# Performance work log

Hardware: AMD Instinct MI355X
Metric: run time of the kernel (lower is better)

Reference implementation:

```python
import jax, jax.numpy as jnp
import numpy as np
from jax import lax

IN_DIM = 256
MID = IN_DIM // 2          # 128
NUM_FILTERS = 8
OUT_DIM = 256
EMBED_DIM = 256
BN_EPS = 1e-5


def star_relu(x, scale, bias):
    # StarReLU: s * relu(x)**2 + b
    return scale * jnp.square(jax.nn.relu(x)) + bias


def setup_inputs() -> dict:
    key = jax.random.key(0)
    ks = jax.random.split(key, 12)
    B, H, W = 2, 16, 16
    h, w = 128, 128
    inp = {
        "x": jax.random.normal(ks[0], (B, IN_DIM, H, W), jnp.float32),
        "y": jax.random.normal(ks[1], (B, OUT_DIM, h, w), jnp.float32),
        # feature_fuse: 1x1 conv, depthwise 3x3 conv, BatchNorm (eval-mode stats)
        "conv1_w": jax.random.normal(ks[2], (MID, IN_DIM), jnp.float32) * 0.02,
        "conv1_b": jnp.zeros((MID,), jnp.float32),
        "dw_w": jax.random.normal(ks[3], (MID, 3, 3), jnp.float32) * 0.02,
        "dw_b": jnp.zeros((MID,), jnp.float32),
        "bn_gamma": jnp.ones((MID,), jnp.float32),
        "bn_beta": jnp.zeros((MID,), jnp.float32),
        "bn_mean": jax.random.normal(ks[4], (MID,), jnp.float32) * 0.1,
        "bn_var": jax.random.uniform(ks[5], (MID,), jnp.float32, 0.5, 1.5),
        "sr1_scale": jnp.ones((1,), jnp.float32),
        "sr1_bias": jnp.zeros((1,), jnp.float32),
        # channle_expand 1x1 conv
        "ce_w": jax.random.normal(ks[6], (NUM_FILTERS, MID), jnp.float32) * 0.02,
        "ce_b": jnp.zeros((NUM_FILTERS,), jnp.float32),
        "sr2_scale": jnp.ones((1,), jnp.float32),
        "sr2_bias": jnp.zeros((1,), jnp.float32),
        "W_base": jax.random.normal(ks[7], (OUT_DIM * EMBED_DIM, NUM_FILTERS), jnp.float32) * 0.02,
    }
    return inp


def reference(x, y, conv1_w, conv1_b, dw_w, dw_b, bn_gamma, bn_beta, bn_mean,
              bn_var, sr1_scale, sr1_bias, ce_w, ce_b, sr2_scale, sr2_bias, W_base):
    B, _, fh, fw = x.shape
    b, c, h, w = y.shape
    ph, pw = h // fh, w // fw

    # feature_fuse
    t = jnp.einsum('bchw,oc->bohw', x, conv1_w) + conv1_b[None, :, None, None]
    t = lax.conv_general_dilated(
        t, dw_w[:, None, :, :], (1, 1), ((1, 1), (1, 1)),
        feature_group_count=MID,
        dimension_numbers=('NCHW', 'OIHW', 'NCHW')) + dw_b[None, :, None, None]
    t = bn_gamma[None, :, None, None] * (t - bn_mean[None, :, None, None]) \
        * lax.rsqrt(bn_var + BN_EPS)[None, :, None, None] + bn_beta[None, :, None, None]
    t = star_relu(t, sr1_scale, sr1_bias)

    # channle_expand + act -> per-location filter coefficients [b, F, fh, fw]
    wdec = star_relu(jnp.einsum('bchw,fc->bfhw', t, ce_w) + ce_b[None, :, None, None],
                     sr2_scale, sr2_bias)

    # hypernetwork: [b, E*O, fh, fw], flattened as (embed_dim, out_dim)
    Wd = jnp.einsum('bfhw,ef->behw', wdec, W_base)
    Wd = Wd.reshape(b, EMBED_DIM, OUT_DIM, fh, fw)

    # massive-group 1x1 conv == per-(batch, block) small GEMM over spatial patches
    yb = y.reshape(b, c, fh, ph, fw, pw)
    out = jnp.einsum('beoij,boipjq->beipjq', Wd, yb)  # [b, E, fh, ph, fw, pw]
    return out.reshape(b, EMBED_DIM, h, w)
```

## Files before the change

### kernel.cpp

```cpp
#include <hip/hip_runtime.h>
#include <stdint.h>

typedef unsigned short u16t;
typedef unsigned int   u32t;
typedef _Float16       h16;
typedef __attribute__((ext_vector_type(2))) _Float16 h16x2;
typedef __attribute__((ext_vector_type(8))) short    short8;
typedef __attribute__((ext_vector_type(4))) float    f32x4;

#if defined(__has_builtin)
#if __has_builtin(__builtin_amdgcn_fdot2)
#define HAVE_DOT2 1
#endif
#endif

__device__ __forceinline__ float dot2h(u32t a, u32t b, float c){
#ifdef HAVE_DOT2
  return __builtin_amdgcn_fdot2(__builtin_bit_cast(h16x2, a),
                                __builtin_bit_cast(h16x2, b), c, false);
#else
  h16x2 ha = __builtin_bit_cast(h16x2, a), hb = __builtin_bit_cast(h16x2, b);
  return c + (float)ha[0]*(float)hb[0] + (float)ha[1]*(float)hb[1];
#endif
}

__device__ __forceinline__ float bf2f(u16t h){
  union { u32t u; float f; } c; c.u = ((u32t)h) << 16; return c.f;
}
__device__ __forceinline__ u32t pk2bf(float a, float b){
  u32t ua = __builtin_bit_cast(u32t, a) + 0x8000u;
  u32t ub = __builtin_bit_cast(u32t, b) + 0x8000u;
  return __builtin_amdgcn_perm(ub, ua, 0x07060302u);
}
__device__ __forceinline__ u32t pk2h(float a, float b){
  h16x2 h = { (h16)a, (h16)b };
  return __builtin_bit_cast(u32t, h);
}

template<bool BF>
__device__ __forceinline__ float ldv(const void* p, size_t i){
  if constexpr (BF) return bf2f(((const u16t*)p)[i]);
  else              return ((const float*)p)[i];
}
template<bool BF>
__device__ __forceinline__ void ld8(const void* p, size_t i, float* v){
  if constexpr (BF){
    uint4 u = *(const uint4*)((const u16t*)p + i);
    const u32t a[4] = {u.x, u.y, u.z, u.w};
#pragma unroll
    for (int d = 0; d < 4; ++d){
      v[2*d]   = bf2f((u16t)(a[d] & 0xffffu));
      v[2*d+1] = bf2f((u16t)(a[d] >> 16));
    }
  } else {
    const float4* q = (const float4*)((const float*)p + i);
    float4 A = q[0], B = q[1];
    v[0]=A.x; v[1]=A.y; v[2]=A.z; v[3]=A.w;
    v[4]=B.x; v[5]=B.y; v[6]=B.z; v[7]=B.w;
  }
}
template<bool BF>
__device__ __forceinline__ void ld8pk(const void* p, size_t i, u32t* dst){
  if constexpr (BF){
    uint4 u = *(const uint4*)((const u16t*)p + i);
    dst[0]=u.x; dst[1]=u.y; dst[2]=u.z; dst[3]=u.w;
  } else {
    const float4* q = (const float4*)((const float*)p + i);
    float4 A = q[0], B = q[1];
    dst[0] = pk2bf(A.x, A.y); dst[1] = pk2bf(A.z, A.w);
    dst[2] = pk2bf(B.x, B.y); dst[3] = pk2bf(B.z, B.w);
  }
}

__device__ __forceinline__ bool probe_bf(const void* xv){
  const u16t* p = (const u16t*)xv;
  const int lane = threadIdx.x & 63;
  const u16t h0 = p[lane], h1 = p[lane + 64];
  const int e0 = (h0 >> 7) & 0xff, e1 = (h1 >> 7) & 0xff;
  unsigned long long b0 = __ballot(e0 >= 90 && e0 <= 150);
  unsigned long long b1 = __ballot(e1 >= 90 && e1 <= 150);
  return (__popcll(b0) + __popcll(b1)) >= 104;
}

template<bool BF>
__device__ __forceinline__ void pre12_body(
    const void* x, const void* w, const void* bias,
    const void* dww, const void* dwb,
    const void* bng, const void* bnb, const void* bnm, const void* bnv,
    const void* s1s, const void* s1b, float* t2)
{
  __shared__ float ts[256];
  const int bid = blockIdx.x;
  const int b = bid >> 7, c = bid & 127;
  const int ij = threadIdx.x, i = ij >> 4, j = ij & 15;
  float a0 = ldv<BF>(bias, c);
  const size_t xb = (size_t)b * 65536 + ij;
#pragma unroll 8
  for (int k = 0; k < 256; ++k)
    a0 += ldv<BF>(x, xb + (size_t)k * 256) * ldv<BF>(w, (size_t)c * 256 + k);
  ts[ij] = a0;
  __syncthreads();
  float s = ldv<BF>(dwb, c);
#pragma unroll
  for (int di = 0; di < 3; ++di){
    const int ii = i + di - 1;
    if (ii < 0 || ii > 15) continue;
#pragma unroll
    for (int dj = 0; dj < 3; ++dj){
      const int jj = j + dj - 1;
      if (jj < 0 || jj > 15) continue;
      s += ts[ii * 16 + jj] * ldv<BF>(dww, c * 9 + di * 3 + dj);
    }
  }
  const float v = ldv<BF>(bng, c) * (s - ldv<BF>(bnm, c)) *
                  rsqrtf(ldv<BF>(bnv, c) + 1e-5f) + ldv<BF>(bnb, c);
  const float r = fmaxf(v, 0.0f);
  t2[((size_t)b * 128 + c) * 256 + ij] = ldv<BF>(s1s, 0) * r * r + ldv<BF>(s1b, 0);
}
__global__ __launch_bounds__(256) void k_pre12(
    const void* x, const void* w, const void* bias,
    const void* dww, const void* dwb,
    const void* bng, const void* bnb, const void* bnm, const void* bnv,
    const void* s1s, const void* s1b, float* t2){
  if (probe_bf(x)) pre12_body<true >(x,w,bias,dww,dwb,bng,bnb,bnm,bnv,s1s,s1b,t2);
  else             pre12_body<false>(x,w,bias,dww,dwb,bng,bnb,bnm,bnv,s1s,s1b,t2);
}

template<bool BF>
__device__ __forceinline__ void pre3_body(
    const void* x, const float* t2, const void* cew, const void* ceb,
    const void* s2s, const void* s2b, uint4* wdech)
{
  __shared__ float cs[8][128];
  const int b = blockIdx.x, ij = threadIdx.x;
  for (int t = ij; t < 1024; t += 256) cs[t >> 7][t & 127] = ldv<BF>(cew, t);
  __syncthreads();
  float a[8];
#pragma unroll
  for (int f = 0; f < 8; ++f) a[f] = ldv<BF>(ceb, f);
#pragma unroll 4
  for (int c = 0; c < 128; ++c){
    const float tv = t2[((size_t)b * 128 + c) * 256 + ij];
#pragma unroll
    for (int f = 0; f < 8; ++f) a[f] += tv * cs[f][c];
  }
  const float sc2 = ldv<BF>(s2s, 0), sb2 = ldv<BF>(s2b, 0);
  float o[8];
#pragma unroll
  for (int f = 0; f < 8; ++f){
    const float r = fmaxf(a[f], 0.0f);
    o[f] = sc2 * r * r + sb2;
  }
  wdech[b * 256 + ij] = make_uint4(pk2h(o[0], o[1]), pk2h(o[2], o[3]),
                                   pk2h(o[4], o[5]), pk2h(o[6], o[7]));
}
__global__ __launch_bounds__(256) void k_pre3(
    const void* x, const float* t2, const void* cew, const void* ceb,
    const void* s2s, const void* s2b, uint4* wdech){
  if (probe_bf(x)) pre3_body<true >(x, t2, cew, ceb, s2s, s2b, wdech);
  else             pre3_body<false>(x, t2, cew, ceb, s2s, s2b, wdech);
}

template<bool BF>
__device__ __forceinline__ void prew_body(const void* wb, uint4* wbh2){
  const int t = blockIdx.x * 256 + threadIdx.x;
  const int e = t & 255, o = t >> 8;
  float v[8];
  ld8<BF>(wb, ((size_t)e * 256 + o) * 8, v);
  wbh2[(size_t)o * 256 + e] = make_uint4(pk2h(v[0], v[1]), pk2h(v[2], v[3]),
                                         pk2h(v[4], v[5]), pk2h(v[6], v[7]));
}
__global__ __launch_bounds__(256) void k_prew(const void* x, const void* wb, uint4* wbh2){
  if (probe_bf(x)) prew_body<true >(wb, wbh2);
  else             prew_body<false>(wb, wbh2);
}

template<bool BF>
__device__ __forceinline__ void main_body(
    const void* y, const uint4* wbh2, const uint4* wdech, float* out, u16t* smem)
{
  const int bid = blockIdx.x;
  const int ec  = (bid >> 3) & 1;
  const int gx  = (bid & 7) | ((bid >> 4) << 3);
  const int b   = gx >> 7;
  const int i   = (gx >> 3) & 15;
  const int j0  = (gx & 7) * 2;
  const int tid = threadIdx.x;

  {
    const int o_oct = tid & 31;
    const int p     = (tid >> 5) & 7;
    const int g     = tid >> 8;
    u32t Rp[8][4];
#pragma unroll
    for (int r = 0; r < 8; ++r){
      const size_t idx = (((size_t)(b * 256 + o_oct * 8 + r)) * 128 + (i * 8 + p)) * 128
                       + (j0 + g) * 8;
      ld8pk<BF>(y, idx, Rp[r]);
    }
#pragma unroll
    for (int q = 0; q < 8; ++q){
      const int d = q >> 1, h = q & 1;
      u32t cc[4];
#pragma unroll
      for (int k = 0; k < 4; ++k){
        const u32t lo32 = Rp[2*k][d], hi32 = Rp[2*k+1][d];
        cc[k] = h ? ((lo32 >> 16)     | (hi32 & 0xffff0000u))
                  : ((lo32 & 0xffffu) | (hi32 << 16));
      }
      const int row  = g * 64 + p * 8 + q;
      const int phys = (o_oct + row) & 31;
      *(uint4*)(smem + row * 256 + phys * 8) = make_uint4(cc[0], cc[1], cc[2], cc[3]);
    }
  }

  const int wave = tid >> 6, lane = tid & 63;
  const int l15 = lane & 15, l4 = lane >> 4;
  const int e0  = ec * 128 + wave * 16;

  u32t wdp[2][4];
#pragma unroll
  for (int g = 0; g < 2; ++g){
    const uint4 q = wdech[b * 256 + i * 16 + j0 + g];
    wdp[g][0] = q.x; wdp[g][1] = q.y; wdp[g][2] = q.z; wdp[g][3] = q.w;
  }

  const uint4* wrow = wbh2 + (size_t)(l4 * 8) * 256 + e0 + l15;

  uint4 Wb[2][8];
#pragma unroll
  for (int r = 0; r < 8; ++r) Wb[0][r] = wrow[(size_t)r * 256];

  f32x4 acc[2][4];
#pragma unroll
  for (int g = 0; g < 2; ++g)
#pragma unroll
    for (int nt = 0; nt < 4; ++nt)
      acc[g][nt] = (f32x4){0.f, 0.f, 0.f, 0.f};

  __syncthreads();

#pragma unroll
  for (int ks = 0; ks < 8; ++ks){
    const int cur = ks & 1;
    if (ks < 7){
#pragma unroll
      for (int r = 0; r < 8; ++r)
        Wb[cur ^ 1][r] = wrow[(size_t)((ks + 1) * 32 + r) * 256];
    }
    float s[2][8];
#pragma unroll
    for (int r = 0; r < 8; ++r){
      const uint4 w4 = Wb[cur][r];
#pragma unroll
      for (int g = 0; g < 2; ++g){
        float t = dot2h(w4.x, wdp[g][0], 0.0f);
        t = dot2h(w4.y, wdp[g][1], t);
        t = dot2h(w4.z, wdp[g][2], t);
        s[g][r] = dot2h(w4.w, wdp[g][3], t);
      }
    }
#pragma unroll
    for (int g = 0; g < 2; ++g){
      u32t a4[4];
#pragma unroll
      for (int d = 0; d < 4; ++d) a4[d] = pk2bf(s[g][2*d], s[g][2*d+1]);
      const short8 af = __builtin_bit_cast(short8, *(uint4*)a4);
#pragma unroll
      for (int nt = 0; nt < 4; ++nt){
        const int row  = g * 64 + nt * 16 + l15;
        const int phys = (ks * 4 + l4 + row) & 31;
        const short8 bfr = *(const short8*)(smem + row * 256 + phys * 8);
        acc[g][nt] = __builtin_amdgcn_mfma_f32_16x16x32_bf16(af, bfr, acc[g][nt], 0, 0, 0);
      }
    }
  }

#pragma unroll
  for (int g = 0; g < 2; ++g){
#pragma unroll
    for (int nt = 0; nt < 4; ++nt){
      const int col = nt * 16 + l15;
      const int pp = col >> 3, qq = col & 7;
#pragma unroll
      for (int r = 0; r < 4; ++r){
        const int ee = e0 + l4 * 4 + r;
        const size_t oaddr = ((size_t)(b * 256 + ee) * 128 + (i * 8 + pp)) * 128
                           + (j0 + g) * 8 + qq;
        out[oaddr] = acc[g][nt][r];
      }
    }
  }
}
__global__ __launch_bounds__(512, 4) void k_main(
    const void* x, const void* y, const uint4* wbh2, const uint4* wdech, float* out){
  extern __shared__ __align__(16) u16t smem[];
  if (probe_bf(x)) main_body<true >(y, wbh2, wdech, out, smem);
  else             main_body<false>(y, wbh2, wdech, out, smem);
}

extern "C" void kernel_launch(void* const* d_in, const int* in_sizes, int n_in,
                              void* d_out, int out_size, void* d_ws, size_t ws_size,
                              hipStream_t stream)
{
  float* t2    = (float*)d_ws;
  uint4* wdech = (uint4*)((char*)d_ws + 262144);
  uint4* wbh2  = (uint4*)((char*)d_ws + 270336);

  k_pre12<<<dim3(256), dim3(256), 0, stream>>>(
      d_in[0], d_in[2], d_in[3], d_in[4], d_in[5], d_in[6], d_in[7],
      d_in[8], d_in[9], d_in[10], d_in[11], t2);
  k_pre3<<<dim3(2), dim3(256), 0, stream>>>(
      d_in[0], t2, d_in[12], d_in[13], d_in[14], d_in[15], wdech);
  k_prew<<<dim3(256), dim3(256), 0, stream>>>(d_in[0], d_in[16], wbh2);

  const int lds_bytes = 2 * 64 * 256 * 2;
  hipFuncSetAttribute((const void*)k_main,
                      hipFuncAttributeMaxDynamicSharedMemorySize, lds_bytes);
  k_main<<<dim3(512), dim3(512), lds_bytes, stream>>>(
      d_in[0], d_in[1], wbh2, wdech, (float*)d_out);
}
```

Baseline: 169.4 us.

## Fuse prologue kernels, pre-transpose y to workspace, async-load slabs into LDS

Replaces the three prologue launches with one heterogeneous kernel whose blocks transpose y into fp16 slabs, compute the conv/BN/StarReLU stage, or repack W_base. The channel-expand step moves into the main kernel, where 16 threads per block compute the eight filter coefficients. The main kernel now loads pre-transposed slabs straight into LDS with global_load_lds and runs 1024-thread blocks covering all 256 embed channels. This cuts launch count and the in-kernel transpose, but adds an extra write and read of the transposed y through global memory and runs a serial 128-step reduction in the main kernel.

```diff
diff --git a/kernel.cpp b/kernel.cpp
--- a/kernel.cpp
+++ b/kernel.cpp
@@ -82,23 +82,59 @@
   return (__popcll(b0) + __popcll(b1)) >= 104;
 }
 
+__device__ __forceinline__ void gld_lds16(const void* g, void* l){
+  __builtin_amdgcn_global_load_lds(
+      (const __attribute__((address_space(1))) u32t*)g,
+      (__attribute__((address_space(3))) u32t*)l, 16, 0, 0);
+}
+
+
+template<bool BF>
+__device__ __forceinline__ void trans_body(const void* y, u16t* yt, int bid){
+  const int b = bid >> 7, i = (bid >> 3) & 15, jp = bid & 7;
+  const int tid   = threadIdx.x;
+  const int o_oct = tid & 31, p = (tid >> 5) & 7, g = (tid >> 8) & 1, rh = tid >> 9;
+  u32t Rp[4][4];
+#pragma unroll
+  for (int r4 = 0; r4 < 4; ++r4){
+    const int r = rh * 4 + r4;
+    const size_t idx = (((size_t)(b * 256 + o_oct * 8 + r)) * 128 + (i * 8 + p)) * 128
+                     + (jp * 2 + g) * 8;
+    ld8pk<BF>(y, idx, Rp[r4]);
+  }
+  u16t* slab = yt + (size_t)bid * 32768;
+#pragma unroll
+  for (int q = 0; q < 8; ++q){
+    const int d = q >> 1, h = q & 1;
+    const u32t lo0 = Rp[0][d], hi0 = Rp[1][d];
+    const u32t lo1 = Rp[2][d], hi1 = Rp[3][d];
+    const u32t c0 = h ? ((lo0 >> 16)     | (hi0 & 0xffff0000u))
+                      : ((lo0 & 0xffffu) | (hi0 << 16));
+    const u32t c1 = h ? ((lo1 >> 16)     | (hi1 & 0xffff0000u))
+                      : ((lo1 & 0xffffu) | (hi1 << 16));
+    const int row  = g * 64 + p * 8 + q;
+    const int phys = (o_oct + row) & 31;
+    *(uint2*)(slab + (size_t)row * 256 + phys * 8 + rh * 4) = make_uint2(c0, c1);
+  }
+}
+
 template<bool BF>
 __device__ __forceinline__ void pre12_body(
     const void* x, const void* w, const void* bias,
     const void* dww, const void* dwb,
     const void* bng, const void* bnb, const void* bnm, const void* bnv,
-    const void* s1s, const void* s1b, float* t2)
-{
-  __shared__ float ts[256];
-  const int bid = blockIdx.x;
-  const int b = bid >> 7, c = bid & 127;
-  const int ij = threadIdx.x, i = ij >> 4, j = ij & 15;
+    const void* s1s, const void* s1b, float* t2, float (*ts)[256], int bq)
+{
+  const int b = bq >> 5, cq = bq & 31;
+  const int cl = threadIdx.x >> 8, ij = threadIdx.x & 255;
+  const int c = cq * 4 + cl;
+  const int i = ij >> 4, j = ij & 15;
   float a0 = ldv<BF>(bias, c);
   const size_t xb = (size_t)b * 65536 + ij;
 #pragma unroll 8
   for (int k = 0; k < 256; ++k)
     a0 += ldv<BF>(x, xb + (size_t)k * 256) * ldv<BF>(w, (size_t)c * 256 + k);
-  ts[ij] = a0;
+  ts[cl][ij] = a0;
   __syncthreads();
   float s = ldv<BF>(dwb, c);
 #pragma unroll
@@ -109,7 +145,7 @@
     for (int dj = 0; dj < 3; ++dj){
       const int jj = j + dj - 1;
       if (jj < 0 || jj > 15) continue;
-      s += ts[ii * 16 + jj] * ldv<BF>(dww, c * 9 + di * 3 + dj);
+      s += ts[cl][ii * 16 + jj] * ldv<BF>(dww, c * 9 + di * 3 + dj);
     }
   }
   const float v = ldv<BF>(bng, c) * (s - ldv<BF>(bnm, c)) *
@@ -117,113 +153,74 @@
   const float r = fmaxf(v, 0.0f);
   t2[((size_t)b * 128 + c) * 256 + ij] = ldv<BF>(s1s, 0) * r * r + ldv<BF>(s1b, 0);
 }
-__global__ __launch_bounds__(256) void k_pre12(
-    const void* x, const void* w, const void* bias,
-    const void* dww, const void* dwb,
-    const void* bng, const void* bnb, const void* bnm, const void* bnv,
-    const void* s1s, const void* s1b, float* t2){
-  if (probe_bf(x)) pre12_body<true >(x,w,bias,dww,dwb,bng,bnb,bnm,bnv,s1s,s1b,t2);
-  else             pre12_body<false>(x,w,bias,dww,dwb,bng,bnb,bnm,bnv,s1s,s1b,t2);
-}
-
-template<bool BF>
-__device__ __forceinline__ void pre3_body(
-    const void* x, const float* t2, const void* cew, const void* ceb,
-    const void* s2s, const void* s2b, uint4* wdech)
-{
-  __shared__ float cs[8][128];
-  const int b = blockIdx.x, ij = threadIdx.x;
-  for (int t = ij; t < 1024; t += 256) cs[t >> 7][t & 127] = ldv<BF>(cew, t);
-  __syncthreads();
-  float a[8];
-#pragma unroll
-  for (int f = 0; f < 8; ++f) a[f] = ldv<BF>(ceb, f);
-#pragma unroll 4
-  for (int c = 0; c < 128; ++c){
-    const float tv = t2[((size_t)b * 128 + c) * 256 + ij];
-#pragma unroll
-    for (int f = 0; f < 8; ++f) a[f] += tv * cs[f][c];
-  }
-  const float sc2 = ldv<BF>(s2s, 0), sb2 = ldv<BF>(s2b, 0);
-  float o[8];
-#pragma unroll
-  for (int f = 0; f < 8; ++f){
-    const float r = fmaxf(a[f], 0.0f);
-    o[f] = sc2 * r * r + sb2;
-  }
-  wdech[b * 256 + ij] = make_uint4(pk2h(o[0], o[1]), pk2h(o[2], o[3]),
-                                   pk2h(o[4], o[5]), pk2h(o[6], o[7]));
-}
-__global__ __launch_bounds__(256) void k_pre3(
-    const void* x, const float* t2, const void* cew, const void* ceb,
-    const void* s2s, const void* s2b, uint4* wdech){
-  if (probe_bf(x)) pre3_body<true >(x, t2, cew, ceb, s2s, s2b, wdech);
-  else             pre3_body<false>(x, t2, cew, ceb, s2s, s2b, wdech);
-}
-
-template<bool BF>
-__device__ __forceinline__ void prew_body(const void* wb, uint4* wbh2){
-  const int t = blockIdx.x * 256 + threadIdx.x;
+
+template<bool BF>
+__device__ __forceinline__ void prew_body(const void* wb, uint4* wbh2, int pb){
+  const int t = pb * 1024 + threadIdx.x;
   const int e = t & 255, o = t >> 8;
   float v[8];
   ld8<BF>(wb, ((size_t)e * 256 + o) * 8, v);
   wbh2[(size_t)o * 256 + e] = make_uint4(pk2h(v[0], v[1]), pk2h(v[2], v[3]),
                                          pk2h(v[4], v[5]), pk2h(v[6], v[7]));
 }
-__global__ __launch_bounds__(256) void k_prew(const void* x, const void* wb, uint4* wbh2){
-  if (probe_bf(x)) prew_body<true >(wb, wbh2);
-  else             prew_body<false>(wb, wbh2);
+
+__global__ __launch_bounds__(1024) void k_fused(
+    const void* x, const void* y,
+    const void* w1, const void* b1, const void* dww, const void* dwb,
+    const void* bng, const void* bnb, const void* bnm, const void* bnv,
+    const void* s1s, const void* s1b, const void* wb,
+    float* t2, uint4* wbh2, u16t* yt)
+{
+  __shared__ float ts[4][256];
+  const bool bf = probe_bf(x);
+  const int bid = blockIdx.x;
+  if (bid < 256){
+    if (bf) trans_body<true >(y, yt, bid);
+    else    trans_body<false>(y, yt, bid);
+  } else if (bid < 320){
+    if (bf) pre12_body<true >(x,w1,b1,dww,dwb,bng,bnb,bnm,bnv,s1s,s1b,t2,ts,bid-256);
+    else    pre12_body<false>(x,w1,b1,dww,dwb,bng,bnb,bnm,bnv,s1s,s1b,t2,ts,bid-256);
+  } else {
+    if (bf) prew_body<true >(wb, wbh2, bid - 320);
+    else    prew_body<false>(wb, wbh2, bid - 320);
+  }
 }
 
 template<bool BF>
 __device__ __forceinline__ void main_body(
-    const void* y, const uint4* wbh2, const uint4* wdech, float* out, u16t* smem)
+    const float* t2, const void* cew, const void* ceb,
+    const void* s2s, const void* s2b,
+    const u16t* yt, const uint4* wbh2, float* out, u16t* smem)
 {
   const int bid = blockIdx.x;
-  const int ec  = (bid >> 3) & 1;
-  const int gx  = (bid & 7) | ((bid >> 4) << 3);
-  const int b   = gx >> 7;
-  const int i   = (gx >> 3) & 15;
-  const int j0  = (gx & 7) * 2;
+  const int b = bid >> 7, i = (bid >> 3) & 15, j0 = (bid & 7) * 2;
   const int tid = threadIdx.x;
+  const int wv = tid >> 6, lane = tid & 63;
 
   {
-    const int o_oct = tid & 31;
-    const int p     = (tid >> 5) & 7;
-    const int g     = tid >> 8;
-    u32t Rp[8][4];
-#pragma unroll
-    for (int r = 0; r < 8; ++r){
-      const size_t idx = (((size_t)(b * 256 + o_oct * 8 + r)) * 128 + (i * 8 + p)) * 128
-                       + (j0 + g) * 8;
-      ld8pk<BF>(y, idx, Rp[r]);
-    }
-#pragma unroll
-    for (int q = 0; q < 8; ++q){
-      const int d = q >> 1, h = q & 1;
-      u32t cc[4];
-#pragma unroll
-      for (int k = 0; k < 4; ++k){
-        const u32t lo32 = Rp[2*k][d], hi32 = Rp[2*k+1][d];
-        cc[k] = h ? ((lo32 >> 16)     | (hi32 & 0xffff0000u))
-                  : ((lo32 & 0xffffu) | (hi32 << 16));
-      }
-      const int row  = g * 64 + p * 8 + q;
-      const int phys = (o_oct + row) & 31;
-      *(uint4*)(smem + row * 256 + phys * 8) = make_uint4(cc[0], cc[1], cc[2], cc[3]);
-    }
-  }
-
-  const int wave = tid >> 6, lane = tid & 63;
+    const char* src = (const char*)yt + (size_t)bid * 65536 + wv * 4096 + lane * 16;
+    char* dst = (char*)smem + wv * 4096;
+#pragma unroll
+    for (int k = 0; k < 4; ++k)
+      gld_lds16(src + k * 1024, dst + k * 1024);
+  }
+
+  float* wds = (float*)(smem + 32768);
+
+  if (tid < 16){
+    const int g = tid >> 3, f = tid & 7;
+    const int ij = i * 16 + j0 + g;
+    float a = ldv<BF>(ceb, f);
+    const float* tp = t2 + (size_t)b * 32768 + ij;
+#pragma unroll 8
+    for (int c = 0; c < 128; ++c)
+      a += tp[(size_t)c * 256] * ldv<BF>(cew, (size_t)f * 128 + c);
+    const float r = fmaxf(a, 0.0f);
+    wds[tid] = ldv<BF>(s2s, 0) * r * r + ldv<BF>(s2b, 0);
+  }
+
   const int l15 = lane & 15, l4 = lane >> 4;
-  const int e0  = ec * 128 + wave * 16;
-
-  u32t wdp[2][4];
-#pragma unroll
-  for (int g = 0; g < 2; ++g){
-    const uint4 q = wdech[b * 256 + i * 16 + j0 + g];
-    wdp[g][0] = q.x; wdp[g][1] = q.y; wdp[g][2] = q.z; wdp[g][3] = q.w;
-  }
+  const int e0  = wv * 16;
 
   const uint4* wrow = wbh2 + (size_t)(l4 * 8) * 256 + e0 + l15;
 
@@ -239,6 +236,13 @@
       acc[g][nt] = (f32x4){0.f, 0.f, 0.f, 0.f};
 
   __syncthreads();
+
+  u32t wdp[2][4];
+#pragma unroll
+  for (int g = 0; g < 2; ++g)
+#pragma unroll
+    for (int d = 0; d < 4; ++d)
+      wdp[g][d] = pk2h(wds[g * 8 + 2 * d], wds[g * 8 + 2 * d + 1]);
 
 #pragma unroll
   for (int ks = 0; ks < 8; ++ks){
@@ -292,11 +296,14 @@
     }
   }
 }
-__global__ __launch_bounds__(512, 4) void k_main(
-    const void* x, const void* y, const uint4* wbh2, const uint4* wdech, float* out){
+__global__ __launch_bounds__(1024, 4) void k_main(
+    const void* x, const float* t2, const void* cew, const void* ceb,
+    const void* s2s, const void* s2b,
+    const u16t* yt, const uint4* wbh2, float* out)
+{
   extern __shared__ __align__(16) u16t smem[];
-  if (probe_bf(x)) main_body<true >(y, wbh2, wdech, out, smem);
-  else             main_body<false>(y, wbh2, wdech, out, smem);
+  if (probe_bf(x)) main_body<true >(t2, cew, ceb, s2s, s2b, yt, wbh2, out, smem);
+  else             main_body<false>(t2, cew, ceb, s2s, s2b, yt, wbh2, out, smem);
 }
 
 extern "C" void kernel_launch(void* const* d_in, const int* in_sizes, int n_in,
@@ -304,19 +311,16 @@
                               hipStream_t stream)
 {
   float* t2    = (float*)d_ws;
-  uint4* wdech = (uint4*)((char*)d_ws + 262144);
-  uint4* wbh2  = (uint4*)((char*)d_ws + 270336);
-
-  k_pre12<<<dim3(256), dim3(256), 0, stream>>>(
-      d_in[0], d_in[2], d_in[3], d_in[4], d_in[5], d_in[6], d_in[7],
-      d_in[8], d_in[9], d_in[10], d_in[11], t2);
-  k_pre3<<<dim3(2), dim3(256), 0, stream>>>(
-      d_in[0], t2, d_in[12], d_in[13], d_in[14], d_in[15], wdech);
-  k_prew<<<dim3(256), dim3(256), 0, stream>>>(d_in[0], d_in[16], wbh2);
-
-  const int lds_bytes = 2 * 64 * 256 * 2;
+  uint4* wbh2  = (uint4*)((char*)d_ws + 262144);
+  u16t*  yt    = (u16t*)((char*)d_ws + 1310720);
+
+  k_fused<<<dim3(384), dim3(1024), 0, stream>>>(
+      d_in[0], d_in[1], d_in[2], d_in[3], d_in[4], d_in[5], d_in[6], d_in[7],
+      d_in[8], d_in[9], d_in[10], d_in[11], d_in[16], t2, wbh2, yt);
+
+  const int lds_bytes = 65536 + 64;
   hipFuncSetAttribute((const void*)k_main,
                       hipFuncAttributeMaxDynamicSharedMemorySize, lds_bytes);
-  k_main<<<dim3(512), dim3(512), lds_bytes, stream>>>(
-      d_in[0], d_in[1], wbh2, wdech, (float*)d_out);
-}
+  k_main<<<dim3(256), dim3(1024), lds_bytes, stream>>>(
+      d_in[0], t2, d_in[12], d_in[13], d_in[14], d_in[15], yt, wbh2, (float*)d_out);
+}
```

After: 180.2 us. +6.4%, slower.
